# Kernel tuning notes

Hardware: AMD Instinct MI355X
Metric: run time of the kernel (lower is better)

Reference implementation:

```python
import jax, jax.numpy as jnp
import numpy as np

E, H, D, T, B = 768, 12, 64, 2048, 2
HID = 4 * E

def _layernorm(x, g, b, eps=1e-5):
    mu = jnp.mean(x, axis=-1, keepdims=True)
    var = jnp.mean(jnp.square(x - mu), axis=-1, keepdims=True)
    return (x - mu) * jax.lax.rsqrt(var + eps) * g + b

def setup_inputs() -> dict:
    key = jax.random.key(0)
    ks = jax.random.split(key, 8)
    s = 0.02
    return {
        "x": jax.random.normal(ks[0], (B, T, E), jnp.float32),
        "Wq": jax.random.normal(ks[1], (H, E, D), jnp.float32) * s,
        "Wk": jax.random.normal(ks[2], (H, E, D), jnp.float32) * s,
        "Wv": jax.random.normal(ks[3], (H, E, D), jnp.float32) * s,
        "W1": jax.random.normal(ks[4], (E, HID), jnp.float32) * s,
        "b1": jnp.zeros((HID,), jnp.float32),
        "W2": jax.random.normal(ks[5], (HID, E), jnp.float32) * s,
        "b2": jnp.zeros((E,), jnp.float32),
        "ln1_g": jnp.ones((E,), jnp.float32),
        "ln1_b": jnp.zeros((E,), jnp.float32),
        "ln2_g": jnp.ones((E,), jnp.float32),
        "ln2_b": jnp.zeros((E,), jnp.float32),
    }

def reference(x, Wq, Wk, Wv, W1, b1, W2, b2, ln1_g, ln1_b, ln2_g, ln2_b):
    b, t, e = x.shape
    # per-head projections (stacked): [B,H,T,D]
    q = jnp.einsum('bte,hed->bhtd', x, Wq)
    k = jnp.einsum('bte,hed->bhtd', x, Wk)
    v = jnp.einsum('bte,hed->bhtd', x, Wv)
    scores = jnp.einsum('bhtd,bhsd->bhts', q, k) / jnp.sqrt(jnp.float32(D))
    causal = jnp.tril(jnp.ones((t, t), bool))
    masked = jnp.where(causal, scores, -jnp.inf)
    p = jax.nn.softmax(masked, axis=-1)
    av = jnp.einsum('bhts,bhsd->bhtd', p, v)  # [B,H,T,D]
    attn_out = av.transpose(0, 2, 1, 3).reshape(b, t, e)  # concat heads
    y = _layernorm(x + attn_out, ln1_g, ln1_b)
    mlp = jnp.maximum(y @ W1 + b1, 0.0) @ W2 + b2
    return _layernorm(y + mlp, ln2_g, ln2_b)
```

## Files before the change

kernel.cpp:

```cpp
#include <hip/hip_runtime.h>
#include <stdint.h>

constexpr int Ee   = 768;
constexpr int Hh   = 12;
constexpr int Dd   = 64;
constexpr int Tt   = 2048;
constexpr int Bb   = 2;
constexpr int HIDc = 3072;
constexpr int MROWS = Bb * Tt;
constexpr int NQKV  = 3 * Hh * Dd;

typedef unsigned short u16;
typedef __bf16 bf16;
typedef bf16 bf16x8 __attribute__((ext_vector_type(8)));
typedef float f32x4 __attribute__((ext_vector_type(4)));
typedef float f32x16 __attribute__((ext_vector_type(16)));

__device__ __forceinline__ u16 f2bf(float f) {
  uint32_t u = __builtin_bit_cast(uint32_t, f);
  u += 0x7fffu + ((u >> 16) & 1u);
  return (u16)(u >> 16);
}

__device__ __forceinline__ float bf2f(u16 v) {
  uint32_t u = (uint32_t)v << 16;
  return __builtin_bit_cast(float, u);
}

__device__ __forceinline__ uint32_t cvt_pk_bf16(float lo, float hi) {
  uint32_t r;
  asm("v_cvt_pk_bf16_f32 %0, %1, %2" : "=v"(r) : "v"(lo), "v"(hi));
  return r;
}

__device__ __forceinline__ f32x4 mfma16(bf16x8 a, bf16x8 b, f32x4 c) {
  return __builtin_amdgcn_mfma_f32_16x16x32_bf16(a, b, c, 0, 0, 0);
}

__device__ __forceinline__ f32x16 mfma32(bf16x8 a, bf16x8 b, f32x16 c) {
  return __builtin_amdgcn_mfma_f32_32x32x16_bf16(a, b, c, 0, 0, 0);
}

#define GLOAD_LDS16(gp, lp)                                                            \
  __builtin_amdgcn_global_load_lds((const __attribute__((address_space(1))) void*)(gp),\
                                   (__attribute__((address_space(3))) void*)(lp),      \
                                   16, 0, 0)

#define KSWZ(row, byte) ((row) * 128 + ((byte) ^ (((row) & 7) << 4)))


__device__ __forceinline__ void tr_body(const float* __restrict__ ip,
                                        u16* __restrict__ op,
                                        int R, int C, int r0, int c0,
                                        float (*t)[33]) {
  const int tx = threadIdx.x & 31, ty = threadIdx.x >> 5;
#pragma unroll
  for (int i = 0; i < 4; ++i)
    t[ty * 4 + i][tx] = ip[(size_t)(r0 + ty * 4 + i) * C + c0 + tx];
  __syncthreads();
#pragma unroll
  for (int i = 0; i < 4; ++i)
    op[(size_t)(c0 + ty * 4 + i) * R + r0 + tx] = f2bf(t[tx][ty * 4 + i]);
}

__global__ __launch_bounds__(256) void prep_kernel(
    const float* __restrict__ x, u16* __restrict__ xb,
    const float* __restrict__ Wq, const float* __restrict__ Wk,
    const float* __restrict__ Wv, u16* __restrict__ wqkvt,
    const float* __restrict__ W1, u16* __restrict__ w1t,
    const float* __restrict__ W2, u16* __restrict__ w2t) {
  __shared__ float t[32][33];
  int bid = blockIdx.x;
  if (bid < 3072) {
    const int i = bid * 256 + threadIdx.x;
    const float4 f = *(const float4*)(x + (size_t)i * 4);
    uint2 o;
    u16* po = (u16*)&o;
    po[0] = f2bf(f.x); po[1] = f2bf(f.y); po[2] = f2bf(f.z); po[3] = f2bf(f.w);
    *(uint2*)(xb + (size_t)i * 4) = o;
    return;
  }
  bid -= 3072;
  if (bid < 1728) {
    const int bx = bid & 1;
    const int rest = bid >> 1;
    const int by = rest % 24, z = rest / 24;
    const int which = z / 12, hs = z - which * 12;
    const float* W = (which == 0) ? Wq : (which == 1) ? Wk : Wv;
    tr_body(W + (size_t)hs * Ee * Dd, wqkvt + ((size_t)which * 768 + hs * 64) * Ee,
            Ee, Dd, by * 32, bx * 32, t);
    return;
  }
  bid -= 1728;
  if (bid < 2304) {
    const int bx = bid % 96, by = bid / 96;
    tr_body(W1, w1t, Ee, HIDc, by * 32, bx * 32, t);
    return;
  }
  bid -= 2304;
  {
    const int bx = bid % 24, by = bid / 24;
    tr_body(W2, w2t, HIDc, Ee, by * 32, bx * 32, t);
  }
}

template <int EPI, int BN, int SPLITK>
__global__ __launch_bounds__(256) void gemm_bt_kernel(
    const u16* __restrict__ A, const u16* __restrict__ Bt,
    const float* __restrict__ bias,
    u16* __restrict__ out_u, u16* __restrict__ out_p,
    u16* __restrict__ qp, u16* __restrict__ kp, u16* __restrict__ vp,
    int Mdim, int Ndim, int Kdim, int gx, int gy) {
  constexpr int WN = BN / 64;
  constexpr int WM = 4 / WN;
  constexpr int MR = 128 / WM / 16;
  constexpr int ACH = 16;
  constexpr int BCH = BN / 8;
  __shared__ u16 la[2][128 * 64];
  __shared__ u16 lb[2][BN * 64];
  const int tid = threadIdx.x, lane = tid & 63, wv = tid >> 6;
  const int wm = wv / WN, wn = wv % WN;
  const int l15 = lane & 15, l4 = lane >> 4;

  const int nwg = gx * gy * SPLITK;
  const int cpx = nwg >> 3;
  const int wg = (blockIdx.x & 7) * cpx + (blockIdx.x >> 3);
  const int bx = wg % gx;
  const int byz = wg / gx;
  const int by = byz % gy;
  const int kz = byz / gy;
  const int m0 = by * 128, n0 = bx * BN;
  const int Ks = Kdim / SPLITK;
  const int kbase = kz * Ks;
  const int niter = Ks / 64;

  auto stage = [&](int it, int buf) {
    const int k0 = kbase + it * 64;
#pragma unroll
    for (int j = 0; j < ACH / 4; ++j) {
      const int cb = (wv * (ACH / 4) + j) * 64;
      const int ci = cb + lane;
      const int row = ci >> 3;
      const int kbl = ((ci & 7) * 16) ^ ((row & 7) << 4);
      GLOAD_LDS16(A + (size_t)(m0 + row) * Kdim + k0 + (kbl >> 1), la[buf] + (size_t)cb * 8);
    }
#pragma unroll
    for (int j = 0; j < BCH / 4; ++j) {
      const int cb = (wv * (BCH / 4) + j) * 64;
      const int ci = cb + lane;
      const int row = ci >> 3;
      const int kbl = ((ci & 7) * 16) ^ ((row & 7) << 4);
      GLOAD_LDS16(Bt + (size_t)(n0 + row) * Kdim + k0 + (kbl >> 1), lb[buf] + (size_t)cb * 8);
    }
  };

  f32x4 acc[MR][4] = {};
  stage(0, 0);

  for (int it = 0; it < niter; ++it) {
    __syncthreads();
    const int cur = it & 1;
    if (it + 1 < niter) stage(it + 1, cur ^ 1);
    const char* lac = (const char*)la[cur];
    const char* lbc = (const char*)lb[cur];
#pragma unroll
    for (int ks = 0; ks < 2; ++ks) {
      bf16x8 af[MR], bfr[4];
#pragma unroll
      for (int i = 0; i < MR; ++i) {
        const int row = wm * (MR * 16) + i * 16 + l15;
        af[i] = *(const bf16x8*)(lac + row * 128 +
                                 (((ks * 64 + l4 * 16)) ^ ((row & 7) << 4)));
      }
#pragma unroll
      for (int i = 0; i < 4; ++i) {
        const int row = wn * 64 + i * 16 + l15;
        bfr[i] = *(const bf16x8*)(lbc + row * 128 +
                                  (((ks * 64 + l4 * 16)) ^ ((row & 7) << 4)));
      }
      __builtin_amdgcn_s_setprio(1);
#pragma unroll
      for (int mi = 0; mi < MR; ++mi)
#pragma unroll
        for (int ni = 0; ni < 4; ++ni)
          acc[mi][ni] = mfma16(af[mi], bfr[ni], acc[mi][ni]);
      __builtin_amdgcn_s_setprio(0);
    }
  }

#pragma unroll
  for (int mi = 0; mi < MR; ++mi)
#pragma unroll
    for (int ni = 0; ni < 4; ++ni) {
      const int mb = m0 + wm * (MR * 16) + mi * 16 + l4 * 4;
      const int n = n0 + wn * 64 + ni * 16 + l15;
      if constexpr (EPI == 0) {
        const int b = mb >> 11, tb = mb & 2047;
        const int which = n / (Hh * Dd);
        const int nn = n - which * (Hh * Dd);
        const int h = nn >> 6, d = nn & 63;
        if (which == 2) {
          uint2 pw;
          pw.x = cvt_pk_bf16(acc[mi][ni][0], acc[mi][ni][1]);
          pw.y = cvt_pk_bf16(acc[mi][ni][2], acc[mi][ni][3]);
          const int tp = (tb & ~15) | ((tb & 4) << 1) | ((tb & 8) >> 1);
          *(uint2*)(vp + ((size_t)(b * Hh + h) * Dd + d) * Tt + tp) = pw;
        } else {
          u16* dst = (which == 0) ? qp : kp;
#pragma unroll
          for (int r = 0; r < 4; ++r)
            dst[((size_t)(b * Hh + h) * Tt + tb + r) * Dd + d] = f2bf(acc[mi][ni][r]);
        }
      } else if constexpr (EPI == 1) {
#pragma unroll
        for (int r = 0; r < 4; ++r) {
          float val = acc[mi][ni][r] + bias[n];
          val = fmaxf(val, 0.0f);
          out_u[(size_t)(mb + r) * Ndim + n] = f2bf(val);
        }
      } else {
#pragma unroll
        for (int r = 0; r < 4; ++r) {
          float val = acc[mi][ni][r];
          if (kz == 0) val += bias[n];
          out_p[(size_t)kz * Mdim * Ndim + (size_t)(mb + r) * Ndim + n] = f2bf(val);
        }
      }
    }
}

__global__ __launch_bounds__(256) void attn_kernel(const u16* __restrict__ q,
                                                   const u16* __restrict__ k,
                                                   const u16* __restrict__ vtg,
                                                   u16* __restrict__ Pb,
                                                   float* __restrict__ Lb) {
  __shared__ u16 kl[2][64 * 64];
  __shared__ u16 vt[2][64 * 64];
  const int tid = threadIdx.x, lane = tid & 63, w = tid >> 6;
  const int l31 = lane & 31, hi = lane >> 5;
  const int bid = blockIdx.x;
  const int x8 = bid & 7, r3 = bid >> 3;
  const int g = r3 % 3, u = r3 / 3;
  int q128, c, nt;
  if (u < 4)       { q128 = 15; c = u; nt = 8; }
  else if (u < 16) { const int v = u - 4;  q128 = 14 - v / 3; c = v % 3; nt = 8; }
  else if (u < 24) { const int v = u - 16; q128 = 10 - v / 2; c = v % 2; nt = 8; }
  else if (u < 28) { q128 = 6 - (u - 24); c = 0; nt = 8; }
  else             { const int v = u - 28; const int row = v >> 2, col = v & 3;
                     nt = 6 - 2 * row; q128 = 14 - row - 4 * col; c = 3 - col; }
  const int ts0 = c * 8;
  const int bh = g * 8 + x8;
  const int wq = 2 * q128 + (w >> 1);
  const int tg = q128 * 128 + (w >> 1) * 64 + (w & 1) * 32 + l31;
  constexpr float SC = 0.18033688f;

  const u16* kgb = k + (size_t)bh * Tt * Dd;
  const u16* vgb = vtg + (size_t)bh * Dd * Tt;

  bf16x8 qf[4];
#pragma unroll
  for (int kt = 0; kt < 4; ++kt)
    qf[kt] = *(const bf16x8*)(q + ((size_t)bh * Tt + tg) * Dd + kt * 16 + hi * 8);

  {
    const int sb0 = ts0 * 64;
#pragma unroll
    for (int jj = 0; jj < 2; ++jj) {
      const int cb = (w * 2 + jj) * 64;
      const int ci = cb + lane;
      const int row = ci >> 3;
      const int sb = ((ci & 7) * 16) ^ ((row & 7) << 4);
      GLOAD_LDS16(kgb + (size_t)(sb0 + row) * Dd + (sb >> 1), kl[0] + (size_t)cb * 8);
      GLOAD_LDS16(vgb + (size_t)row * Tt + sb0 + (sb >> 1), vt[0] + (size_t)cb * 8);
    }
  }

  f32x16 oacc0 = {}, oacc1 = {};
  float lrun = 0.f;

  for (int jt = 0; jt < nt; ++jt) {
    __syncthreads();
    const int cur = jt & 1;
    if (jt + 1 < nt) {
      const int s0n = (ts0 + jt + 1) * 64;
#pragma unroll
      for (int jj = 0; jj < 2; ++jj) {
        const int cb = (w * 2 + jj) * 64;
        const int ci = cb + lane;
        const int row = ci >> 3;
        const int sb = ((ci & 7) * 16) ^ ((row & 7) << 4);
        GLOAD_LDS16(kgb + (size_t)(s0n + row) * Dd + (sb >> 1), kl[cur ^ 1] + (size_t)cb * 8);
        GLOAD_LDS16(vgb + (size_t)row * Tt + s0n + (sb >> 1), vt[cur ^ 1] + (size_t)cb * 8);
      }
    }
    const int tile = ts0 + jt;
    if (tile <= wq) {
      const u16* klc = kl[cur];
      const u16* vtc = vt[cur];

      f32x16 sacc0 = {}, sacc1 = {};
      __builtin_amdgcn_s_setprio(1);
#pragma unroll
      for (int kt = 0; kt < 4; ++kt) {
        const int b0 = kt * 32 + hi * 16;
        const bf16x8 kf0 = *(const bf16x8*)((const char*)klc + KSWZ(l31, b0));
        const bf16x8 kf1 = *(const bf16x8*)((const char*)klc + KSWZ(32 + l31, b0));
        sacc0 = mfma32(kf0, qf[kt], sacc0);
        sacc1 = mfma32(kf1, qf[kt], sacc1);
      }
      __builtin_amdgcn_s_setprio(0);

      const bool diag = (tile == wq);
      bf16x8 pf[4];
      float rs = 0.f;
#pragma unroll
      for (int sh = 0; sh < 2; ++sh) {
        const f32x16 sa = sh ? sacc1 : sacc0;
#pragma unroll
        for (int kt2 = 0; kt2 < 2; ++kt2) {
          float p8[8];
#pragma unroll
          for (int o = 0; o < 8; ++o) {
            const int r = kt2 * 8 + o;
            float e = __builtin_amdgcn_exp2f(sa[r] * SC);
            if (diag) {
              const int sg = tile * 64 + sh * 32 + kt2 * 16 + (o & 3) + 8 * (o >> 2) + 4 * hi;
              e = (sg > tg) ? 0.f : e;
            }
            p8[o] = e;
            rs += e;
          }
          uint4 uu;
          uu.x = cvt_pk_bf16(p8[0], p8[1]);
          uu.y = cvt_pk_bf16(p8[2], p8[3]);
          uu.z = cvt_pk_bf16(p8[4], p8[5]);
          uu.w = cvt_pk_bf16(p8[6], p8[7]);
          pf[sh * 2 + kt2] = __builtin_bit_cast(bf16x8, uu);
        }
      }
      lrun += rs;

      __builtin_amdgcn_s_setprio(1);
#pragma unroll
      for (int ks = 0; ks < 4; ++ks) {
        const int b0 = ks * 32 + hi * 16;
        const bf16x8 vf0 = *(const bf16x8*)((const char*)vtc + KSWZ(l31, b0));
        const bf16x8 vf1 = *(const bf16x8*)((const char*)vtc + KSWZ(32 + l31, b0));
        oacc0 = mfma32(vf0, pf[ks], oacc0);
        oacc1 = mfma32(vf1, pf[ks], oacc1);
      }
      __builtin_amdgcn_s_setprio(0);
    }
  }

  const float lt = lrun + __shfl_xor(lrun, 32);
  const int b = bh / Hh, h = bh - (bh / Hh) * Hh;
  u16* orow = Pb + (size_t)c * MROWS * Ee + ((size_t)b * Tt + tg) * Ee + h * Dd;
#pragma unroll
  for (int dt = 0; dt < 2; ++dt) {
    const f32x16 oa = dt ? oacc1 : oacc0;
#pragma unroll
    for (int kq = 0; kq < 4; ++kq) {
      uint2 pw;
      pw.x = cvt_pk_bf16(oa[4 * kq + 0], oa[4 * kq + 1]);
      pw.y = cvt_pk_bf16(oa[4 * kq + 2], oa[4 * kq + 3]);
      *(uint2*)(orow + dt * 32 + 8 * kq + 4 * hi) = pw;
    }
  }
  if (hi == 0)
    Lb[(size_t)c * MROWS * 12 + ((size_t)b * Tt + tg) * 12 + h] = lt;
}

__global__ __launch_bounds__(256) void ln1_kernel(const float* __restrict__ x,
                                                  const u16* __restrict__ P,
                                                  const float* __restrict__ L,
                                                  const float* __restrict__ g,
                                                  const float* __restrict__ beta,
                                                  u16* __restrict__ ybout) {
  const int w = threadIdx.x >> 6, lane = threadIdx.x & 63;
  const int m = blockIdx.x * 4 + w;
  const int t = m & (Tt - 1);
  float inv = 0.f;
  if (lane < 12) {
    float s = L[(size_t)m * 12 + lane];
    if (t >= 512)  s += L[(size_t)(1 * MROWS + m) * 12 + lane];
    if (t >= 1024) s += L[(size_t)(2 * MROWS + m) * 12 + lane];
    if (t >= 1536) s += L[(size_t)(3 * MROWS + m) * 12 + lane];
    inv = 1.0f / s;
  }
  float vbuf[12];
  float s = 0.f, ss = 0.f;
#pragma unroll
  for (int j = 0; j < 3; ++j) {
    const int e = j * 256 + lane * 4;
    const float ih = __shfl(inv, 4 * j + (lane >> 4));
    float o[4];
    {
      const uint2 p0 = *(const uint2*)(P + (size_t)m * Ee + e);
      const u16* pp = (const u16*)&p0;
#pragma unroll
      for (int r = 0; r < 4; ++r) o[r] = bf2f(pp[r]);
    }
    if (t >= 512) {
      const uint2 p1 = *(const uint2*)(P + (size_t)(1 * MROWS + m) * Ee + e);
      const u16* pp = (const u16*)&p1;
#pragma unroll
      for (int r = 0; r < 4; ++r) o[r] += bf2f(pp[r]);
    }
    if (t >= 1024) {
      const uint2 p2 = *(const uint2*)(P + (size_t)(2 * MROWS + m) * Ee + e);
      const u16* pp = (const u16*)&p2;
#pragma unroll
      for (int r = 0; r < 4; ++r) o[r] += bf2f(pp[r]);
    }
    if (t >= 1536) {
      const uint2 p3 = *(const uint2*)(P + (size_t)(3 * MROWS + m) * Ee + e);
      const u16* pp = (const u16*)&p3;
#pragma unroll
      for (int r = 0; r < 4; ++r) o[r] += bf2f(pp[r]);
    }
    const float4 xv = *(const float4*)(x + (size_t)m * Ee + e);
    const float xr[4] = {xv.x, xv.y, xv.z, xv.w};
#pragma unroll
    for (int r = 0; r < 4; ++r) {
      const float tv = xr[r] + o[r] * ih;
      vbuf[j * 4 + r] = tv;
      s += tv;
      ss += tv * tv;
    }
  }
#pragma unroll
  for (int off = 1; off < 64; off <<= 1) {
    s += __shfl_xor(s, off);
    ss += __shfl_xor(ss, off);
  }
  const float mu = s / Ee;
  const float var = ss / Ee - mu * mu;
  const float rinv = rsqrtf(var + 1e-5f);
#pragma unroll
  for (int j = 0; j < 3; ++j) {
    const int e = j * 256 + lane * 4;
    const float4 gv = *(const float4*)(g + e);
    const float4 bv = *(const float4*)(beta + e);
    const float t0 = (vbuf[j * 4 + 0] - mu) * rinv * gv.x + bv.x;
    const float t1 = (vbuf[j * 4 + 1] - mu) * rinv * gv.y + bv.y;
    const float t2 = (vbuf[j * 4 + 2] - mu) * rinv * gv.z + bv.z;
    const float t3 = (vbuf[j * 4 + 3] - mu) * rinv * gv.w + bv.w;
    uint2 pw;
    pw.x = cvt_pk_bf16(t0, t1);
    pw.y = cvt_pk_bf16(t2, t3);
    *(uint2*)(ybout + (size_t)m * Ee + e) = pw;
  }
}

__global__ __launch_bounds__(256) void ln2_kernel(const u16* __restrict__ a,
                                                  const u16* __restrict__ mlp,
                                                  const float* __restrict__ g,
                                                  const float* __restrict__ beta,
                                                  float* __restrict__ yout) {
  const int w = threadIdx.x >> 6, lane = threadIdx.x & 63;
  const int m = blockIdx.x * 4 + w;
  float vbuf[12];
  float s = 0.f, ss = 0.f;
#pragma unroll
  for (int j = 0; j < 3; ++j) {
    const int e = j * 256 + lane * 4;
    float o[4];
    {
      const uint2 p0 = *(const uint2*)(a + (size_t)m * Ee + e);
      const u16* pp = (const u16*)&p0;
#pragma unroll
      for (int r = 0; r < 4; ++r) o[r] = bf2f(pp[r]);
    }
#pragma unroll
    for (int kz = 0; kz < 2; ++kz) {
      const uint2 p1 = *(const uint2*)(mlp + (size_t)(kz * MROWS + m) * Ee + e);
      const u16* pp = (const u16*)&p1;
#pragma unroll
      for (int r = 0; r < 4; ++r) o[r] += bf2f(pp[r]);
    }
#pragma unroll
    for (int r = 0; r < 4; ++r) {
      vbuf[j * 4 + r] = o[r];
      s += o[r];
      ss += o[r] * o[r];
    }
  }
#pragma unroll
  for (int off = 1; off < 64; off <<= 1) {
    s += __shfl_xor(s, off);
    ss += __shfl_xor(ss, off);
  }
  const float mu = s / Ee;
  const float var = ss / Ee - mu * mu;
  const float rinv = rsqrtf(var + 1e-5f);
#pragma unroll
  for (int j = 0; j < 3; ++j) {
    const int e = j * 256 + lane * 4;
    const float4 gv = *(const float4*)(g + e);
    const float4 bv = *(const float4*)(beta + e);
    float4 ov;
    ov.x = (vbuf[j * 4 + 0] - mu) * rinv * gv.x + bv.x;
    ov.y = (vbuf[j * 4 + 1] - mu) * rinv * gv.y + bv.y;
    ov.z = (vbuf[j * 4 + 2] - mu) * rinv * gv.z + bv.z;
    ov.w = (vbuf[j * 4 + 3] - mu) * rinv * gv.w + bv.w;
    *(float4*)(yout + (size_t)m * Ee + e) = ov;
  }
}

extern "C" void kernel_launch(void* const* d_in, const int* in_sizes, int n_in,
                              void* d_out, int out_size, void* d_ws, size_t ws_size,
                              hipStream_t stream) {
  const float* x  = (const float*)d_in[0];
  const float* Wq = (const float*)d_in[1];
  const float* Wk = (const float*)d_in[2];
  const float* Wv = (const float*)d_in[3];
  const float* W1 = (const float*)d_in[4];
  const float* b1 = (const float*)d_in[5];
  const float* W2 = (const float*)d_in[6];
  const float* b2 = (const float*)d_in[7];
  const float* g1 = (const float*)d_in[8];
  const float* be1 = (const float*)d_in[9];
  const float* g2 = (const float*)d_in[10];
  const float* be2 = (const float*)d_in[11];
  float* out = (float*)d_out;

  char* ws = (char*)d_ws;
  size_t off = 0;
  auto alloc = [&](size_t bytes) -> char* {
    char* p = ws + off;
    off += (bytes + 255) & ~(size_t)255;
    return p;
  };
  u16* xb    = (u16*)alloc((size_t)MROWS * Ee * 2);
  u16* wqkvt = (u16*)alloc((size_t)NQKV * Ee * 2);
  u16* w1t   = (u16*)alloc((size_t)HIDc * Ee * 2);
  u16* w2t   = (u16*)alloc((size_t)Ee * HIDc * 2);
  u16* qb    = (u16*)alloc((size_t)Bb * Hh * Tt * Dd * 2);
  u16* kb    = (u16*)alloc((size_t)Bb * Hh * Tt * Dd * 2);
  u16* vtb   = (u16*)alloc((size_t)Bb * Hh * Tt * Dd * 2);
  u16* yb     = (u16*)alloc((size_t)MROWS * Ee * 2);
  float* Lb   = (float*)alloc((size_t)4 * MROWS * 12 * 4);
  char* big = alloc((size_t)MROWS * HIDc * 2 + (size_t)2 * MROWS * Ee * 2);
  u16* Pb    = (u16*)big;
  u16* hbuf  = (u16*)big;
  u16* mlp   = (u16*)(big + (size_t)MROWS * HIDc * 2);
  (void)ws_size;

  prep_kernel<<<9408, 256, 0, stream>>>(x, xb, Wq, Wk, Wv, wqkvt, W1, w1t, W2, w2t);

  gemm_bt_kernel<0, 64, 1><<<36 * 32, 256, 0, stream>>>(
      xb, wqkvt, nullptr, nullptr, nullptr, qb, kb, vtb, MROWS, NQKV, Ee, 36, 32);

  attn_kernel<<<960, 256, 0, stream>>>(qb, kb, vtb, Pb, Lb);

  ln1_kernel<<<MROWS / 4, 256, 0, stream>>>(x, Pb, Lb, g1, be1, yb);

  gemm_bt_kernel<1, 64, 1><<<48 * 32, 256, 0, stream>>>(
      yb, w1t, b1, hbuf, nullptr, nullptr, nullptr, nullptr, MROWS, HIDc, Ee, 48, 32);
  gemm_bt_kernel<2, 64, 2><<<12 * 32 * 2, 256, 0, stream>>>(
      hbuf, w2t, b2, nullptr, mlp, nullptr, nullptr, nullptr, MROWS, Ee, HIDc, 12, 32);

  ln2_kernel<<<MROWS / 4, 256, 0, stream>>>(yb, mlp, g2, be2, out);
}
```

Before: 143.0 us.

## Move W1/W2 transpose into attention kernel tail and read bf16 x in LN1

The W1/W2 fp32-to-bf16 transpose blocks move from the prep kernel into extra blocks appended to the attention launch, so the transpose can fill idle CUs during the imbalanced causal attention tail. The prep kernel shrinks to the x conversion and QKV weight transpose. LN1 now reads the bf16 copy of x instead of fp32 x, which halves that read but rounds the residual input to bf16 and may cost accuracy. Extra blocks in the attention grid could compete with attention blocks for CUs depending on dispatch order.

New measurement: 138.2 us, median of 2. 3.4% less time.

```diff
diff --git a/kernel.cpp b/kernel.cpp
--- a/kernel.cpp
+++ b/kernel.cpp
@@ -66,9 +66,7 @@
 __global__ __launch_bounds__(256) void prep_kernel(
     const float* __restrict__ x, u16* __restrict__ xb,
     const float* __restrict__ Wq, const float* __restrict__ Wk,
-    const float* __restrict__ Wv, u16* __restrict__ wqkvt,
-    const float* __restrict__ W1, u16* __restrict__ w1t,
-    const float* __restrict__ W2, u16* __restrict__ w2t) {
+    const float* __restrict__ Wv, u16* __restrict__ wqkvt) {
   __shared__ float t[32][33];
   int bid = blockIdx.x;
   if (bid < 3072) {
@@ -81,7 +79,7 @@
     return;
   }
   bid -= 3072;
-  if (bid < 1728) {
+  {
     const int bx = bid & 1;
     const int rest = bid >> 1;
     const int by = rest % 24, z = rest / 24;
@@ -89,18 +87,6 @@
     const float* W = (which == 0) ? Wq : (which == 1) ? Wk : Wv;
     tr_body(W + (size_t)hs * Ee * Dd, wqkvt + ((size_t)which * 768 + hs * 64) * Ee,
             Ee, Dd, by * 32, bx * 32, t);
-    return;
-  }
-  bid -= 1728;
-  if (bid < 2304) {
-    const int bx = bid % 96, by = bid / 96;
-    tr_body(W1, w1t, Ee, HIDc, by * 32, bx * 32, t);
-    return;
-  }
-  bid -= 2304;
-  {
-    const int bx = bid % 24, by = bid / 24;
-    tr_body(W2, w2t, HIDc, Ee, by * 32, bx * 32, t);
   }
 }
 
@@ -233,12 +219,29 @@
                                                    const u16* __restrict__ k,
                                                    const u16* __restrict__ vtg,
                                                    u16* __restrict__ Pb,
-                                                   float* __restrict__ Lb) {
+                                                   float* __restrict__ Lb,
+                                                   const float* __restrict__ W1,
+                                                   u16* __restrict__ w1t,
+                                                   const float* __restrict__ W2,
+                                                   u16* __restrict__ w2t) {
   __shared__ u16 kl[2][64 * 64];
   __shared__ u16 vt[2][64 * 64];
+  const int bid = blockIdx.x;
+  if (bid >= 960) {
+    float (*tt)[33] = (float(*)[33])kl;
+    int b2 = bid - 960;
+    if (b2 < 2304) {
+      const int bx = b2 % 96, by = b2 / 96;
+      tr_body(W1, w1t, Ee, HIDc, by * 32, bx * 32, tt);
+    } else {
+      b2 -= 2304;
+      const int bx = b2 % 24, by = b2 / 24;
+      tr_body(W2, w2t, HIDc, Ee, by * 32, bx * 32, tt);
+    }
+    return;
+  }
   const int tid = threadIdx.x, lane = tid & 63, w = tid >> 6;
   const int l31 = lane & 31, hi = lane >> 5;
-  const int bid = blockIdx.x;
   const int x8 = bid & 7, r3 = bid >> 3;
   const int g = r3 % 3, u = r3 / 3;
   int q128, c, nt;
@@ -371,7 +374,7 @@
     Lb[(size_t)c * MROWS * 12 + ((size_t)b * Tt + tg) * 12 + h] = lt;
 }
 
-__global__ __launch_bounds__(256) void ln1_kernel(const float* __restrict__ x,
+__global__ __launch_bounds__(256) void ln1_kernel(const u16* __restrict__ xb,
                                                   const u16* __restrict__ P,
                                                   const float* __restrict__ L,
                                                   const float* __restrict__ g,
@@ -419,11 +422,11 @@
 #pragma unroll
       for (int r = 0; r < 4; ++r) o[r] += bf2f(pp[r]);
     }
-    const float4 xv = *(const float4*)(x + (size_t)m * Ee + e);
-    const float xr[4] = {xv.x, xv.y, xv.z, xv.w};
+    const uint2 xv = *(const uint2*)(xb + (size_t)m * Ee + e);
+    const u16* xp = (const u16*)&xv;
 #pragma unroll
     for (int r = 0; r < 4; ++r) {
-      const float tv = xr[r] + o[r] * ih;
+      const float tv = bf2f(xp[r]) + o[r] * ih;
       vbuf[j * 4 + r] = tv;
       s += tv;
       ss += tv * tv;
@@ -547,14 +550,14 @@
   u16* mlp   = (u16*)(big + (size_t)MROWS * HIDc * 2);
   (void)ws_size;
 
-  prep_kernel<<<9408, 256, 0, stream>>>(x, xb, Wq, Wk, Wv, wqkvt, W1, w1t, W2, w2t);
+  prep_kernel<<<4800, 256, 0, stream>>>(x, xb, Wq, Wk, Wv, wqkvt);
 
   gemm_bt_kernel<0, 64, 1><<<36 * 32, 256, 0, stream>>>(
       xb, wqkvt, nullptr, nullptr, nullptr, qb, kb, vtb, MROWS, NQKV, Ee, 36, 32);
 
-  attn_kernel<<<960, 256, 0, stream>>>(qb, kb, vtb, Pb, Lb);
-
-  ln1_kernel<<<MROWS / 4, 256, 0, stream>>>(x, Pb, Lb, g1, be1, yb);
+  attn_kernel<<<960 + 4608, 256, 0, stream>>>(qb, kb, vtb, Pb, Lb, W1, w1t, W2, w2t);
+
+  ln1_kernel<<<MROWS / 4, 256, 0, stream>>>(xb, Pb, Lb, g1, be1, yb);
 
   gemm_bt_kernel<1, 64, 1><<<48 * 32, 256, 0, stream>>>(
       yb, w1t, b1, hbuf, nullptr, nullptr, nullptr, nullptr, MROWS, HIDc, Ee, 48, 32);
```
